# Optimization experiments

Measured on AMD Instinct MI355X. Metric: run time of the kernel, lower is better.

## Reference

```python
import jax, jax.numpy as jnp
import numpy as np

D = 384
K = 16
RADII = (1.0, 2.0, 4.0, 8.0)


def layer_norm(x, g, b, eps=1e-5):
    m = jnp.mean(x, axis=-1, keepdims=True)
    v = jnp.var(x, axis=-1, keepdims=True)
    return (x - m) * jax.lax.rsqrt(v + eps) * g + b


def fps(pos, M):
    # Farthest point sampling: deterministic start at index 0. pos: (N,3) -> (M,) int indices.
    dmin0 = jnp.sum((pos - pos[0]) ** 2, axis=-1)

    def step(dmin, _):
        nxt = jnp.argmax(dmin)
        d = jnp.sum((pos - pos[nxt]) ** 2, axis=-1)
        return jnp.minimum(dmin, d), nxt

    _, rest = jax.lax.scan(step, dmin0, None, length=M - 1)
    return jnp.concatenate([jnp.zeros((1,), rest.dtype), rest])


def sa_stage(x, pos, r, lw, lb, sw, dw, pw1, pb1, pw2, pb2, aw, ab, lg, lbt):
    # One set-abstraction stage for a single point cloud. x:(N,D), pos:(N,3).
    N = x.shape[0]
    M = N // 4  # ratio = 0.25
    idx = fps(pos, M)
    q_pos = pos[idx]  # (M,3)
    # k-nearest neighbors within radius r (radius grouping)
    d2 = jnp.sum((q_pos[:, None, :] - pos[None, :, :]) ** 2, axis=-1)  # (M,N)
    neg_d, nbr = jax.lax.top_k(-d2, K)  # (M,K) nearest sources
    valid = (-neg_d) <= r * r  # (M,K); self point (dist 0) always valid
    # PointTransformerConv
    v = x @ lw + lb        # lin (value path)
    a_src = x @ sw         # lin_src, no bias
    a_dst = x[idx] @ dw    # lin_dst, no bias
    rel = q_pos[:, None, :] - pos[nbr]  # (M,K,3)  pos_i - pos_j
    delta = jax.nn.relu(jax.nn.relu(rel @ pw1 + pb1) @ pw2 + pb2)  # pos_nn, (M,K,D)
    alpha = jax.nn.relu((a_dst[:, None, :] - a_src[nbr] + delta) @ aw + ab)  # attn_nn
    alpha = jnp.where(valid[:, :, None], alpha, -1e30)
    attn = jax.nn.softmax(alpha, axis=1) * valid[:, :, None]  # per-dst, per-channel softmax
    out = jnp.sum(attn * (v[nbr] + delta), axis=1)  # (M,D) weighted aggregation
    return layer_norm(out, lg, lbt), q_pos


def setup_inputs() -> dict:
    key = jax.random.key(0)
    ks = jax.random.split(key, 8)
    B, N = 4, 4096
    s = 0.05
    inp = {"pts": jax.random.normal(ks[0], (B, N, 3 + D), jnp.float32)}
    inp["lin_w"] = jax.random.normal(ks[1], (4, D, D), jnp.float32) * s
    inp["lin_b"] = jnp.zeros((4, D), jnp.float32)
    inp["src_w"] = jax.random.normal(ks[2], (4, D, D), jnp.float32) * s
    inp["dst_w"] = jax.random.normal(ks[3], (4, D, D), jnp.float32) * s
    inp["pos_w1"] = jax.random.normal(ks[4], (4, 3, D), jnp.float32) * s
    inp["pos_b1"] = jnp.zeros((4, D), jnp.float32)
    inp["pos_w2"] = jax.random.normal(ks[5], (4, D, D), jnp.float32) * s
    inp["pos_b2"] = jnp.zeros((4, D), jnp.float32)
    inp["attn_w"] = jax.random.normal(ks[6], (4, D, D), jnp.float32) * s
    inp["attn_b"] = jnp.zeros((4, D), jnp.float32)
    inp["ln_g"] = jnp.ones((4, D), jnp.float32)
    inp["ln_b"] = jnp.zeros((4, D), jnp.float32)
    inp["proj_w"] = jax.random.normal(ks[7], (D, D), jnp.float32) * s
    inp["proj_b"] = jnp.zeros((D,), jnp.float32)
    inp["pln_g"] = jnp.ones((D,), jnp.float32)
    inp["pln_b"] = jnp.zeros((D,), jnp.float32)
    return inp


def reference(pts, lin_w, lin_b, src_w, dst_w, pos_w1, pos_b1, pos_w2, pos_b2,
              attn_w, attn_b, ln_g, ln_b, proj_w, proj_b, pln_g, pln_b):
    pos = pts[..., :3]
    x = pts[..., 3:]  # in_proj is Identity (in_dim == out_dim)
    for s in range(4):
        stage_fn = lambda xx, pp, s=s: sa_stage(
            xx, pp, RADII[s], lin_w[s], lin_b[s], src_w[s], dst_w[s],
            pos_w1[s], pos_b1[s], pos_w2[s], pos_b2[s], attn_w[s], attn_b[s],
            ln_g[s], ln_b[s])
        x, pos = jax.vmap(stage_fn)(x, pos)
    feat = layer_norm(x @ proj_w + proj_b, pln_g, pln_b)
    pad = jnp.zeros(feat.shape[:2], dtype=bool)  # ~pad_mask: all points valid
    return pos, feat, pad
```

## Files before the change

### kernel.cpp

```cpp
#include <hip/hip_runtime.h>
#include <math.h>


using half8 = __attribute__((ext_vector_type(8))) _Float16;
using f32x4 = __attribute__((ext_vector_type(4))) float;

__device__ __forceinline__ float d2f(float ax, float ay, float az,
                                     float bx, float by, float bz)
{
  const float dx = __fsub_rn(ax, bx);
  const float dy = __fsub_rn(ay, by);
  const float dz = __fsub_rn(az, bz);
  return __fadd_rn(__fadd_rn(__fmul_rn(dx, dx), __fmul_rn(dy, dy)),
                   __fmul_rn(dz, dz));
}

template<int CTRL>
__device__ __forceinline__ unsigned dppmax_step(unsigned v)
{
  const unsigned o = (unsigned)__builtin_amdgcn_update_dpp(
      (int)v, (int)v, CTRL, 0xF, 0xF, false);
  return o > v ? o : v;
}
__device__ __forceinline__ unsigned wave_max_bcast(unsigned v)
{
  v = dppmax_step<0x111>(v);
  v = dppmax_step<0x112>(v);
  v = dppmax_step<0x114>(v);
  v = dppmax_step<0x118>(v);
  v = dppmax_step<0x142>(v);
  v = dppmax_step<0x143>(v);
  return (unsigned)__builtin_amdgcn_readlane((int)v, 63);
}

__global__ __launch_bounds__(128) void split_kernel(
    const float* __restrict__ pts, float* __restrict__ pos0, float* __restrict__ x0)
{
  const int n = blockIdx.x;
  const int b = blockIdx.y;
  const float* src = pts + ((long)b * 4096 + n) * 387;
  float* pd = pos0 + ((long)b * 4096 + n) * 3;
  float* xd = x0 + ((long)b * 4096 + n) * 384;
  for (int e = threadIdx.x; e < 387; e += 128) {
    float v = src[e];
    if (e < 3) pd[e] = v; else xd[e - 3] = v;
  }
}

struct TP { const float* src[5]; _Float16* dst; };
__global__ __launch_bounds__(256) void transpose_kernel(TP p)
{
  const int z = blockIdx.z;
  const float* S = p.src[z >> 2] + (long)(z & 3) * 147456;
  _Float16* Dst = p.dst + (long)z * 147456;
  const int k0 = blockIdx.x * 32, n0 = blockIdx.y * 32;
  __shared__ float tile[32][33];
  const int ti = threadIdx.x & 31, tj = threadIdx.x >> 5;
  #pragma unroll
  for (int p8 = 0; p8 < 32; p8 += 8)
    tile[tj + p8][ti] = S[(long)(k0 + tj + p8) * 384 + n0 + ti];
  __syncthreads();
  #pragma unroll
  for (int p8 = 0; p8 < 32; p8 += 8)
    Dst[(long)(n0 + tj + p8) * 384 + k0 + ti] = (_Float16)tile[ti][tj + p8];
}

template<int NPTS, int NTHR>
__global__ __launch_bounds__(NTHR, 1) void fps_kernel(
    const float* __restrict__ pos,
    int* __restrict__ idx_out, float* __restrict__ pos_out)
{
  constexpr int NPT = NPTS / NTHR;
  constexpr int NW = NTHR / 64;
  constexpr int M = NPTS / 4;
  const int b = blockIdx.x;
  pos += (long)b * NPTS * 3; idx_out += (long)b * M; pos_out += (long)b * M * 3;
  const int t = threadIdx.x;

  __shared__ float spx[NPTS], spy[NPTS], spz[NPTS];
  __shared__ unsigned long long s_key[2][NW > 1 ? NW : 1];

  float px[NPT], py[NPT], pz[NPT], dmin[NPT];
  #pragma unroll
  for (int i = 0; i < NPT; i++) {
    const int j = t * NPT + i;
    px[i] = pos[j*3]; py[i] = pos[j*3+1]; pz[i] = pos[j*3+2];
    spx[j] = px[i]; spy[j] = py[i]; spz[j] = pz[i];
  }
  const float sx = pos[0], sy = pos[1], sz = pos[2];
  float bv = 0.f; int bi = 0;
  #pragma unroll
  for (int i = 0; i < NPT; i++) {
    const float dd = d2f(px[i], py[i], pz[i], sx, sy, sz);
    dmin[i] = dd;
    if (i == 0) { bv = dd; bi = 0; }
    else { const bool g = dd > bv; bv = g ? dd : bv; bi = g ? i : bi; }
  }
  if (t == 0) { idx_out[0] = 0; pos_out[0] = sx; pos_out[1] = sy; pos_out[2] = sz; }
  if (NW > 1) __syncthreads();

  for (int m = 1; m < M; ++m) {
    const unsigned myub = __float_as_uint(bv);
    const unsigned wmax = wave_max_bcast(myub);
    const unsigned long long mk = __ballot(myub == wmax);
    const int srclane = __builtin_ctzll(mk);
    const int lbi = __shfl(bi, srclane);
    const int wj = ((t & ~63) + srclane) * NPT + lbi;

    int sel;
    if (NW > 1) {
      const int p = m & 1;
      if ((t & 63) == 0)
        s_key[p][t >> 6] =
            ((unsigned long long)wmax << 32) | (unsigned)(NPTS - 1 - wj);
      __syncthreads();
      unsigned long long kb = s_key[p][0];
      #pragma unroll
      for (int w2 = 1; w2 < NW; w2++) {
        const unsigned long long o = s_key[p][w2];
        if (o > kb) kb = o;
      }
      sel = NPTS - 1 - (int)(kb & 0xFFFFFFFFu);
    } else {
      sel = wj;
    }
    const float qx = spx[sel], qy = spy[sel], qz = spz[sel];
    if (t == 0) { idx_out[m] = sel; pos_out[m*3] = qx; pos_out[m*3+1] = qy; pos_out[m*3+2] = qz; }
    float nbv = 0.f; int nbi = 0;
    #pragma unroll
    for (int i = 0; i < NPT; i++) {
      const float dd = d2f(px[i], py[i], pz[i], qx, qy, qz);
      const float nd = fminf(dmin[i], dd);
      dmin[i] = nd;
      if (i == 0) { nbv = nd; nbi = 0; }
      else { const bool g = nd > nbv; nbv = g ? nd : nbv; nbi = g ? i : nbi; }
    }
    bv = nbv; bi = nbi;
  }
}

template<int C>
__global__ __launch_bounds__(64) void knn_kernel(
    const float* __restrict__ pos, const float* __restrict__ qpos,
    int N, int M, int* __restrict__ nbr, float* __restrict__ vld, float r2)
{
  const int m = blockIdx.x, b = blockIdx.y;
  pos += (long)b * N * 3; qpos += (long)b * M * 3;
  nbr += (long)b * (1024 * 16); vld += (long)b * (1024 * 16);
  const int lane = threadIdx.x;
  const float qx = qpos[m*3], qy = qpos[m*3+1], qz = qpos[m*3+2];
  unsigned long long key[C];
  #pragma unroll
  for (int c = 0; c < C; c++) {
    const int j = c * 64 + lane;
    const float dd = d2f(pos[j*3], pos[j*3+1], pos[j*3+2], qx, qy, qz);
    key[c] = ((unsigned long long)__float_as_uint(dd) << 32) | (unsigned)j;
  }
  unsigned long long prev = 0;
  for (int k = 0; k < 16; k++) {
    unsigned long long best = ~0ull;
    #pragma unroll
    for (int c = 0; c < C; c++) {
      const bool take = (k == 0) || (key[c] > prev);
      if (take && key[c] < best) best = key[c];
    }
    #pragma unroll
    for (int off = 32; off; off >>= 1) {
      const unsigned long long o = __shfl_xor(best, off);
      if (o < best) best = o;
    }
    prev = best;
    if (lane == 0) {
      nbr[m*16+k] = (int)(best & 0xFFFFFFFFu);
      const float dd = __uint_as_float((unsigned)(best >> 32));
      vld[m*16+k] = (dd <= r2) ? 1.0f : 0.0f;
    }
  }
}

struct GemmP {
  const float* A; long sA;
  const _Float16* Wt;
  const float* bias;
  float* C; long sC;
  int R;
  const int* gather; long sG;
  const float* qpos; long sQ;
  const float* pos;  long sP;
  const int* nbr;    long sN;
  const float* pw1;
  const float* pb1;
  const float* adst; long sAD;
  const float* asrc; long sAS;
  int row0;
};

template<int AMODE, bool GATHER, bool BIAS, bool RELU>
__global__ __launch_bounds__(256) void mgemm_kernel(GemmP p)
{
  const int b = blockIdx.z;
  const int rb = blockIdx.x * 64;
  const int cb = blockIdx.y * 64;
  const int t = threadIdx.x;
  const float* A = p.A ? (p.A + (long)b * p.sA) : nullptr;
  float* C = p.C + (long)b * p.sC;
  const int* gat = GATHER ? (p.gather + (long)b * p.sG) : nullptr;
  const int* nbrb = (AMODE != 0) ? (p.nbr + (long)b * p.sN) : nullptr;

  __shared__ _Float16 As[64][40];
  __shared__ _Float16 Bs[64][40];

  const int w = t >> 6, lane = t & 63;
  const int wm = w & 1, wn = w >> 1;
  const int quad = lane >> 4, l16 = lane & 15;

  f32x4 acc[2][2] = {};

  const int sr = t >> 2;
  const int sk = (t & 3) << 3;
  const int ar = rb + sr;

  const float* arow = nullptr;
  const float* adrow = nullptr;
  const float* asrow = nullptr;
  bool avalid = true;
  float rx = 0.f, ry = 0.f, rz = 0.f;
  if (AMODE == 0) {
    avalid = (ar < p.R);
    long srcrow = 0;
    if (avalid) srcrow = GATHER ? (long)gat[ar] : (long)ar;
    arow = A + srcrow * 384;
  } else {
    const int grow = p.row0 + ar;
    const int mq = grow >> 4;
    const int n = nbrb[grow];
    if (AMODE == 1) {
      const float* qposb = p.qpos + (long)b * p.sQ;
      const float* posb = p.pos + (long)b * p.sP;
      rx = qposb[mq*3+0] - posb[n*3+0];
      ry = qposb[mq*3+1] - posb[n*3+1];
      rz = qposb[mq*3+2] - posb[n*3+2];
    } else {
      arow = A + (long)ar * 384;
      adrow = p.adst + (long)b * p.sAD + (long)mq * 384;
      asrow = p.asrc + (long)b * p.sAS + (long)n * 384;
    }
  }

  for (int k0 = 0; k0 < 384; k0 += 32) {
    float a8[8];
    if (AMODE == 0) {
      if (avalid) {
        const float4 u = *(const float4*)(arow + k0 + sk);
        const float4 v = *(const float4*)(arow + k0 + sk + 4);
        a8[0]=u.x; a8[1]=u.y; a8[2]=u.z; a8[3]=u.w;
        a8[4]=v.x; a8[5]=v.y; a8[6]=v.z; a8[7]=v.w;
      } else {
        #pragma unroll
        for (int j = 0; j < 8; j++) a8[j] = 0.f;
      }
    } else if (AMODE == 1) {
      const int kc = k0 + sk;
      const float4 w0a = *(const float4*)(p.pw1 + kc);
      const float4 w0b = *(const float4*)(p.pw1 + kc + 4);
      const float4 w1a = *(const float4*)(p.pw1 + 384 + kc);
      const float4 w1b = *(const float4*)(p.pw1 + 384 + kc + 4);
      const float4 w2a = *(const float4*)(p.pw1 + 768 + kc);
      const float4 w2b = *(const float4*)(p.pw1 + 768 + kc + 4);
      const float4 b1a = *(const float4*)(p.pb1 + kc);
      const float4 b1b = *(const float4*)(p.pb1 + kc + 4);
      a8[0] = fmaxf(rx*w0a.x + ry*w1a.x + rz*w2a.x + b1a.x, 0.f);
      a8[1] = fmaxf(rx*w0a.y + ry*w1a.y + rz*w2a.y + b1a.y, 0.f);
      a8[2] = fmaxf(rx*w0a.z + ry*w1a.z + rz*w2a.z + b1a.z, 0.f);
      a8[3] = fmaxf(rx*w0a.w + ry*w1a.w + rz*w2a.w + b1a.w, 0.f);
      a8[4] = fmaxf(rx*w0b.x + ry*w1b.x + rz*w2b.x + b1b.x, 0.f);
      a8[5] = fmaxf(rx*w0b.y + ry*w1b.y + rz*w2b.y + b1b.y, 0.f);
      a8[6] = fmaxf(rx*w0b.z + ry*w1b.z + rz*w2b.z + b1b.z, 0.f);
      a8[7] = fmaxf(rx*w0b.w + ry*w1b.w + rz*w2b.w + b1b.w, 0.f);
    } else {
      const int kc = k0 + sk;
      const float4 d0 = *(const float4*)(arow + kc);
      const float4 d1 = *(const float4*)(arow + kc + 4);
      const float4 a0 = *(const float4*)(adrow + kc);
      const float4 a1 = *(const float4*)(adrow + kc + 4);
      const float4 s0 = *(const float4*)(asrow + kc);
      const float4 s1 = *(const float4*)(asrow + kc + 4);
      a8[0] = a0.x - s0.x + d0.x; a8[1] = a0.y - s0.y + d0.y;
      a8[2] = a0.z - s0.z + d0.z; a8[3] = a0.w - s0.w + d0.w;
      a8[4] = a1.x - s1.x + d1.x; a8[5] = a1.y - s1.y + d1.y;
      a8[6] = a1.z - s1.z + d1.z; a8[7] = a1.w - s1.w + d1.w;
    }
    const half8 bv = *(const half8*)(p.Wt + (long)(cb + sr) * 384 + k0 + sk);

    __syncthreads();
    half8 av;
    #pragma unroll
    for (int j = 0; j < 8; j++) av[j] = (_Float16)a8[j];
    *(half8*)&As[sr][sk] = av;
    *(half8*)&Bs[sr][sk] = bv;
    __syncthreads();

    const half8 fa0 = *(const half8*)&As[wm*32 + l16][quad*8];
    const half8 fa1 = *(const half8*)&As[wm*32 + 16 + l16][quad*8];
    const half8 fb0 = *(const half8*)&Bs[wn*32 + l16][quad*8];
    const half8 fb1 = *(const half8*)&Bs[wn*32 + 16 + l16][quad*8];
    acc[0][0] = __builtin_amdgcn_mfma_f32_16x16x32_f16(fa0, fb0, acc[0][0], 0, 0, 0);
    acc[0][1] = __builtin_amdgcn_mfma_f32_16x16x32_f16(fa0, fb1, acc[0][1], 0, 0, 0);
    acc[1][0] = __builtin_amdgcn_mfma_f32_16x16x32_f16(fa1, fb0, acc[1][0], 0, 0, 0);
    acc[1][1] = __builtin_amdgcn_mfma_f32_16x16x32_f16(fa1, fb1, acc[1][1], 0, 0, 0);
  }

  float bi0 = 0.f, bi1 = 0.f;
  if (BIAS) {
    bi0 = p.bias[cb + wn*32 + l16];
    bi1 = p.bias[cb + wn*32 + 16 + l16];
  }
  #pragma unroll
  for (int i = 0; i < 2; i++) {
    const int base = rb + wm*32 + i*16;
    if (base < p.R) {
      const int r0 = base + quad*4;
      #pragma unroll
      for (int j = 0; j < 2; j++) {
        const int col = cb + wn*32 + j*16 + l16;
        const float bb = j ? bi1 : bi0;
        #pragma unroll
        for (int reg = 0; reg < 4; reg++) {
          float v = acc[i][j][reg] + bb;
          if (RELU) v = fmaxf(v, 0.f);
          C[(long)(r0 + reg) * 384 + col] = v;
        }
      }
    }
  }
}

__global__ __launch_bounds__(128) void attnln_kernel(
    const float* __restrict__ alpha, const float* __restrict__ delta,
    const float* __restrict__ vbuf, const int* __restrict__ nbr,
    const float* __restrict__ vldb, const float* __restrict__ lng,
    const float* __restrict__ lnb, float* __restrict__ xout,
    int q0, long sCh, long sV, long sNb, long sX)
{
  const int ml = blockIdx.x, b = blockIdx.y;
  const int m = q0 + ml;
  alpha += (long)b * sCh; delta += (long)b * sCh; vbuf += (long)b * sV;
  nbr += (long)b * sNb; vldb += (long)b * sNb; xout += (long)b * sX;
  const int t = threadIdx.x;

  int nb[16]; float vl[16];
  #pragma unroll
  for (int k = 0; k < 16; k++) { nb[k] = nbr[m*16+k]; vl[k] = vldb[m*16+k]; }

  const long rbase = (long)ml * 16 * 384;
  float av[16][3];
  #pragma unroll
  for (int k = 0; k < 16; k++)
    #pragma unroll
    for (int i = 0; i < 3; i++) {
      const float a = alpha[rbase + k*384 + t + i*128];
      av[k][i] = (vl[k] > 0.5f) ? a : -1e30f;
    }
  float mx[3] = {-3.4e38f, -3.4e38f, -3.4e38f};
  #pragma unroll
  for (int k = 0; k < 16; k++)
    #pragma unroll
    for (int i = 0; i < 3; i++) mx[i] = fmaxf(mx[i], av[k][i]);
  float sm[3] = {0.f, 0.f, 0.f};
  #pragma unroll
  for (int k = 0; k < 16; k++)
    #pragma unroll
    for (int i = 0; i < 3; i++) { const float e = expf(av[k][i] - mx[i]); av[k][i] = e; sm[i] += e; }
  float rs[3];
  #pragma unroll
  for (int i = 0; i < 3; i++) rs[i] = 1.0f / sm[i];
  float o[3] = {0.f, 0.f, 0.f};
  #pragma unroll
  for (int k = 0; k < 16; k++) {
    const long nrow = (long)nb[k] * 384;
    #pragma unroll
    for (int i = 0; i < 3; i++) {
      const int dd = t + i * 128;
      const float vv = vbuf[nrow + dd] + delta[rbase + k*384 + dd];
      o[i] += (av[k][i] * rs[i] * vl[k]) * vv;
    }
  }
  __shared__ float sred[2];
  float s1 = o[0] + o[1] + o[2];
  #pragma unroll
  for (int off = 32; off; off >>= 1) s1 += __shfl_xor(s1, off);
  if ((t & 63) == 0) sred[t >> 6] = s1;
  __syncthreads();
  const float mean = (sred[0] + sred[1]) * (1.0f / 384.0f);
  __syncthreads();
  float s2 = 0.f;
  #pragma unroll
  for (int i = 0; i < 3; i++) { const float dd = o[i] - mean; s2 += dd * dd; }
  #pragma unroll
  for (int off = 32; off; off >>= 1) s2 += __shfl_xor(s2, off);
  if ((t & 63) == 0) sred[t >> 6] = s2;
  __syncthreads();
  const float var = (sred[0] + sred[1]) * (1.0f / 384.0f);
  const float rstd = 1.0f / sqrtf(var + 1e-5f);
  #pragma unroll
  for (int i = 0; i < 3; i++) {
    const int dd = t + i * 128;
    xout[(long)m * 384 + dd] = (o[i] - mean) * rstd * lng[dd] + lnb[dd];
  }
}

__global__ __launch_bounds__(384) void feat_kernel(
    const float* __restrict__ x4, const float* __restrict__ pw,
    const float* __restrict__ pb, const float* __restrict__ g,
    const float* __restrict__ be, float* __restrict__ outf)
{
  const int row = blockIdx.x, b = blockIdx.y;
  const long r = (long)b * 16 + row;
  const int d = threadIdx.x;
  __shared__ float xs[384];
  xs[d] = x4[r * 384 + d];
  __syncthreads();
  float acc = pb[d];
  #pragma unroll 8
  for (int j = 0; j < 384; j++) acc = fmaf(xs[j], pw[(long)j * 384 + d], acc);
  __shared__ float sred[6];
  float s = acc;
  #pragma unroll
  for (int off = 32; off; off >>= 1) s += __shfl_xor(s, off);
  if ((d & 63) == 0) sred[d >> 6] = s;
  __syncthreads();
  const float mean = (sred[0]+sred[1]+sred[2]+sred[3]+sred[4]+sred[5]) * (1.0f/384.0f);
  __syncthreads();
  float dv = (acc - mean) * (acc - mean);
  #pragma unroll
  for (int off = 32; off; off >>= 1) dv += __shfl_xor(dv, off);
  if ((d & 63) == 0) sred[d >> 6] = dv;
  __syncthreads();
  const float var = (sred[0]+sred[1]+sred[2]+sred[3]+sred[4]+sred[5]) * (1.0f/384.0f);
  const float rstd = 1.0f / sqrtf(var + 1e-5f);
  outf[r * 384 + d] = (acc - mean) * rstd * g[d] + be[d];
}

__global__ void tail_kernel(const float* __restrict__ p4, float* __restrict__ out)
{
  const int t = threadIdx.x;
  if (t < 192) out[t] = p4[t];
  if (t < 64) out[192 + 24576 + t] = 0.0f;
}

extern "C" void kernel_launch(void* const* d_in, const int* in_sizes, int n_in,
                              void* d_out, int out_size, void* d_ws, size_t ws_size,
                              hipStream_t stream)
{
  (void)in_sizes; (void)n_in; (void)out_size; (void)ws_size;
  const float* pts    = (const float*)d_in[0];
  const float* lin_w  = (const float*)d_in[1];
  const float* lin_b  = (const float*)d_in[2];
  const float* src_w  = (const float*)d_in[3];
  const float* dst_w  = (const float*)d_in[4];
  const float* pos_w1 = (const float*)d_in[5];
  const float* pos_b1 = (const float*)d_in[6];
  const float* pos_w2 = (const float*)d_in[7];
  const float* pos_b2 = (const float*)d_in[8];
  const float* attn_w = (const float*)d_in[9];
  const float* attn_b = (const float*)d_in[10];
  const float* ln_g   = (const float*)d_in[11];
  const float* ln_b   = (const float*)d_in[12];
  const float* proj_w = (const float*)d_in[13];
  const float* proj_b = (const float*)d_in[14];
  const float* pln_g  = (const float*)d_in[15];
  const float* pln_b  = (const float*)d_in[16];
  float* out = (float*)d_out;

  constexpr long SX0 = 4096L*384, SX1 = 1024L*384, SX2 = 256L*384, SX3 = 64L*384, SX4 = 16L*384;
  constexpr long SP0 = 4096L*3, SP1 = 1024L*3, SP2 = 256L*3, SP3 = 64L*3, SP4 = 16L*3;
  constexpr long SV  = 4096L*384;
  constexpr long SAD = 1024L*384;
  constexpr long SCH = 4096L*384;
  constexpr long SNB = 1024L*16;

  _Float16* wt = (_Float16*)d_ws;
  float* ws = (float*)(wt + 20L * 147456);
  float* x0 = ws; ws += 4*SX0;
  float* x1 = ws; ws += 4*SX1;
  float* x2 = ws; ws += 4*SX2;
  float* x3 = ws; ws += 4*SX3;
  float* x4 = ws; ws += 4*SX4;
  float* p0 = ws; ws += 4*SP0;
  float* p1 = ws; ws += 4*SP1;
  float* p2 = ws; ws += 4*SP2;
  float* p3 = ws; ws += 4*SP3;
  float* p4 = ws; ws += 4*SP4;
  float* vb = ws; ws += 4*SV;
  float* asb = ws; ws += 4*SV;
  float* adb = ws; ws += 4*SAD;
  float* db = ws; ws += 4*SCH;
  float* ab = ws; ws += 4*SCH;
  float* vld = ws; ws += 4*SNB;
  int* nb = (int*)ws; ws += 4*SNB;
  int* ix[4];
  ix[0] = (int*)ws; ws += 4*1024;
  ix[1] = (int*)ws; ws += 4*256;
  ix[2] = (int*)ws; ws += 4*64;
  ix[3] = (int*)ws; ws += 4*16;

  const int Ns[4] = {4096, 1024, 256, 64};
  const int Ms[4] = {1024, 256, 64, 16};
  const float R2[4] = {1.0f, 4.0f, 16.0f, 64.0f};
  float* X[5] = {x0, x1, x2, x3, x4};
  float* P[5] = {p0, p1, p2, p3, p4};
  long SPs[5] = {SP0, SP1, SP2, SP3, SP4};
  long SXs[5] = {SX0, SX1, SX2, SX3, SX4};

  split_kernel<<<dim3(4096, 4), 128, 0, stream>>>(pts, p0, x0);

  {
    TP tp{};
    tp.src[0] = lin_w; tp.src[1] = src_w; tp.src[2] = dst_w;
    tp.src[3] = pos_w2; tp.src[4] = attn_w;
    tp.dst = wt;
    transpose_kernel<<<dim3(12, 12, 20), 256, 0, stream>>>(tp);
  }

  fps_kernel<4096, 256><<<dim3(4), 256, 0, stream>>>(P[0], ix[0], P[1]);
  fps_kernel<1024, 256><<<dim3(4), 256, 0, stream>>>(P[1], ix[1], P[2]);
  fps_kernel<256, 64><<<dim3(4), 64, 0, stream>>>(P[2], ix[2], P[3]);
  fps_kernel<64, 64><<<dim3(4), 64, 0, stream>>>(P[3], ix[3], P[4]);

  for (int s = 0; s < 4; s++) {
    const int N = Ns[s], M = Ms[s];
    switch (s) {
      case 0: knn_kernel<64><<<dim3(M, 4), 64, 0, stream>>>(P[s], P[s+1], N, M, nb, vld, R2[s]); break;
      case 1: knn_kernel<16><<<dim3(M, 4), 64, 0, stream>>>(P[s], P[s+1], N, M, nb, vld, R2[s]); break;
      case 2: knn_kernel<4><<<dim3(M, 4), 64, 0, stream>>>(P[s], P[s+1], N, M, nb, vld, R2[s]); break;
      default: knn_kernel<1><<<dim3(M, 4), 64, 0, stream>>>(P[s], P[s+1], N, M, nb, vld, R2[s]); break;
    }
    {
      GemmP g{}; g.A = X[s]; g.sA = SXs[s]; g.Wt = wt + (long)(0*4+s)*147456; g.bias = lin_b + (long)s*384;
      g.C = vb; g.sC = SV; g.R = N;
      mgemm_kernel<0, false, true, false><<<dim3(N/64, 6, 4), 256, 0, stream>>>(g);
    }
    {
      GemmP g{}; g.A = X[s]; g.sA = SXs[s]; g.Wt = wt + (long)(1*4+s)*147456;
      g.C = asb; g.sC = SV; g.R = N;
      mgemm_kernel<0, false, false, false><<<dim3(N/64, 6, 4), 256, 0, stream>>>(g);
    }
    {
      GemmP g{}; g.A = X[s]; g.sA = SXs[s]; g.Wt = wt + (long)(2*4+s)*147456;
      g.C = adb; g.sC = SAD; g.R = M; g.gather = ix[s]; g.sG = M;
      mgemm_kernel<0, true, false, false><<<dim3((M+63)/64, 6, 4), 256, 0, stream>>>(g);
    }
    const int nch = (M + 255) / 256;
    for (int c = 0; c < nch; c++) {
      const int q0 = c * 256;
      const int Mc = (M - q0 < 256) ? (M - q0) : 256;
      const int rows = Mc * 16;
      {
        GemmP g{}; g.Wt = wt + (long)(3*4+s)*147456; g.bias = pos_b2 + (long)s*384;
        g.C = db; g.sC = SCH; g.R = rows;
        g.qpos = P[s+1]; g.sQ = SPs[s+1]; g.pos = P[s]; g.sP = SPs[s];
        g.nbr = nb; g.sN = SNB; g.pw1 = pos_w1 + (long)s*1152; g.pb1 = pos_b1 + (long)s*384;
        g.row0 = q0 * 16;
        mgemm_kernel<1, false, true, true><<<dim3(rows/64, 6, 4), 256, 0, stream>>>(g);
      }
      {
        GemmP g{}; g.A = db; g.sA = SCH; g.Wt = wt + (long)(4*4+s)*147456; g.bias = attn_b + (long)s*384;
        g.C = ab; g.sC = SCH; g.R = rows;
        g.nbr = nb; g.sN = SNB; g.adst = adb; g.sAD = SAD; g.asrc = asb; g.sAS = SV;
        g.row0 = q0 * 16;
        mgemm_kernel<2, false, true, true><<<dim3(rows/64, 6, 4), 256, 0, stream>>>(g);
      }
      attnln_kernel<<<dim3(Mc, 4), 128, 0, stream>>>(
          ab, db, vb, nb, vld, ln_g + (long)s*384, ln_b + (long)s*384,
          X[s+1], q0, SCH, SV, SNB, (long)M*384);
    }
  }

  feat_kernel<<<dim3(16, 4), 384, 0, stream>>>(x4, proj_w, proj_b, pln_g, pln_b, out + 192);
  tail_kernel<<<1, 256, 0, stream>>>(p4, out);
}
```

Before: 1.467 ms.

## Co-schedule stage-0 FPS with value and source GEMMs in one fused launch

The stage-0 farthest-point-sampling kernel and the stage-0 lin and lin_src GEMMs are merged into one launch. Block IDs are split so the first four blocks run FPS and the remaining blocks run GEMM tiles, all sharing one static LDS buffer. The long serial FPS, which occupies only four workgroups, can then overlap with the independent GEMM work instead of leaving the GPU mostly idle. In exchange, every block reserves the larger FPS-sized shared memory, which may limit how many GEMM blocks fit per CU.

New measurement: 1.458 ms. About the same (-0.6%).

```diff
diff --git a/kernel.cpp b/kernel.cpp
--- a/kernel.cpp
+++ b/kernel.cpp
@@ -66,19 +66,17 @@
 }
 
 template<int NPTS, int NTHR>
-__global__ __launch_bounds__(NTHR, 1) void fps_kernel(
+__device__ __forceinline__ void fps_body(
     const float* __restrict__ pos,
-    int* __restrict__ idx_out, float* __restrict__ pos_out)
+    int* __restrict__ idx_out, float* __restrict__ pos_out,
+    int b, int t,
+    float* __restrict__ spx, float* __restrict__ spy, float* __restrict__ spz,
+    unsigned long long* __restrict__ s_key)
 {
   constexpr int NPT = NPTS / NTHR;
   constexpr int NW = NTHR / 64;
   constexpr int M = NPTS / 4;
-  const int b = blockIdx.x;
   pos += (long)b * NPTS * 3; idx_out += (long)b * M; pos_out += (long)b * M * 3;
-  const int t = threadIdx.x;
-
-  __shared__ float spx[NPTS], spy[NPTS], spz[NPTS];
-  __shared__ unsigned long long s_key[2][NW > 1 ? NW : 1];
 
   float px[NPT], py[NPT], pz[NPT], dmin[NPT];
   #pragma unroll
@@ -111,13 +109,13 @@
     if (NW > 1) {
       const int p = m & 1;
       if ((t & 63) == 0)
-        s_key[p][t >> 6] =
+        s_key[p*NW + (t >> 6)] =
             ((unsigned long long)wmax << 32) | (unsigned)(NPTS - 1 - wj);
       __syncthreads();
-      unsigned long long kb = s_key[p][0];
+      unsigned long long kb = s_key[p*NW];
       #pragma unroll
       for (int w2 = 1; w2 < NW; w2++) {
-        const unsigned long long o = s_key[p][w2];
+        const unsigned long long o = s_key[p*NW + w2];
         if (o > kb) kb = o;
       }
       sel = NPTS - 1 - (int)(kb & 0xFFFFFFFFu);
@@ -137,6 +135,17 @@
     }
     bv = nbv; bi = nbi;
   }
+}
+
+template<int NPTS, int NTHR>
+__global__ __launch_bounds__(NTHR, 1) void fps_kernel(
+    const float* __restrict__ pos,
+    int* __restrict__ idx_out, float* __restrict__ pos_out)
+{
+  __shared__ float spx[NPTS], spy[NPTS], spz[NPTS];
+  __shared__ unsigned long long s_key[2 * (NTHR > 64 ? NTHR / 64 : 1)];
+  fps_body<NPTS, NTHR>(pos, idx_out, pos_out, blockIdx.x, threadIdx.x,
+                       spx, spy, spz, s_key);
 }
 
 template<int C>
@@ -195,20 +204,19 @@
   int row0;
 };
 
+typedef _Float16 (*H40)[40];
+
 template<int AMODE, bool GATHER, bool BIAS, bool RELU>
-__global__ __launch_bounds__(256) void mgemm_kernel(GemmP p)
-{
-  const int b = blockIdx.z;
-  const int rb = blockIdx.x * 64;
-  const int cb = blockIdx.y * 64;
-  const int t = threadIdx.x;
+__device__ __forceinline__ void mgemm_body(
+    const GemmP& p, int bx, int by, int bz, int t, H40 As, H40 Bs)
+{
+  const int b = bz;
+  const int rb = bx * 64;
+  const int cb = by * 64;
   const float* A = p.A ? (p.A + (long)b * p.sA) : nullptr;
   float* C = p.C + (long)b * p.sC;
   const int* gat = GATHER ? (p.gather + (long)b * p.sG) : nullptr;
   const int* nbrb = (AMODE != 0) ? (p.nbr + (long)b * p.sN) : nullptr;
-
-  __shared__ _Float16 As[64][40];
-  __shared__ _Float16 Bs[64][40];
 
   const int w = t >> 6, lane = t & 63;
   const int wm = w & 1, wn = w >> 1;
@@ -335,6 +343,39 @@
   }
 }
 
+template<int AMODE, bool GATHER, bool BIAS, bool RELU>
+__global__ __launch_bounds__(256) void mgemm_kernel(GemmP p)
+{
+  __shared__ _Float16 As[64][40];
+  __shared__ _Float16 Bs[64][40];
+  mgemm_body<AMODE, GATHER, BIAS, RELU>(p, blockIdx.x, blockIdx.y, blockIdx.z,
+                                        threadIdx.x, As, Bs);
+}
+
+__global__ __launch_bounds__(256) void fat1_kernel(
+    const float* fpos, int* fidx, float* fpout, GemmP gv, GemmP ga)
+{
+  __shared__ char buf[49664] __attribute__((aligned(16)));
+  int bid = blockIdx.x; const int t = threadIdx.x;
+  if (bid < 4) {
+    float* spx = (float*)buf;
+    float* spy = spx + 4096;
+    float* spz = spy + 4096;
+    unsigned long long* s_key = (unsigned long long*)(spz + 4096);
+    fps_body<4096, 256>(fpos, fidx, fpout, bid, t, spx, spy, spz, s_key);
+    return;
+  }
+  bid -= 4;
+  H40 As = (H40)buf;
+  H40 Bs = (H40)(buf + 64 * 40 * sizeof(_Float16));
+  if (bid < 1536) {
+    mgemm_body<0, false, true, false>(gv, bid & 63, (bid >> 6) % 6, bid / 384, t, As, Bs);
+    return;
+  }
+  bid -= 1536;
+  mgemm_body<0, false, false, false>(ga, bid & 63, (bid >> 6) % 6, bid / 384, t, As, Bs);
+}
+
 __global__ __launch_bounds__(128) void attnln_kernel(
     const float* __restrict__ alpha, const float* __restrict__ delta,
     const float* __restrict__ vbuf, const int* __restrict__ nbr,
@@ -522,7 +563,14 @@
     transpose_kernel<<<dim3(12, 12, 20), 256, 0, stream>>>(tp);
   }
 
-  fps_kernel<4096, 256><<<dim3(4), 256, 0, stream>>>(P[0], ix[0], P[1]);
+  {
+    GemmP gv{}; gv.A = x0; gv.sA = SX0; gv.Wt = wt + (long)(0*4+0)*147456;
+    gv.bias = lin_b; gv.C = vb; gv.sC = SV; gv.R = 4096;
+    GemmP ga{}; ga.A = x0; ga.sA = SX0; ga.Wt = wt + (long)(1*4+0)*147456;
+    ga.C = asb; ga.sC = SV; ga.R = 4096;
+    fat1_kernel<<<dim3(4 + 1536 + 1536), 256, 0, stream>>>(p0, ix[0], p1, gv, ga);
+  }
+
   fps_kernel<1024, 256><<<dim3(4), 256, 0, stream>>>(P[1], ix[1], P[2]);
   fps_kernel<256, 64><<<dim3(4), 64, 0, stream>>>(P[2], ix[2], P[3]);
   fps_kernel<64, 64><<<dim3(4), 64, 0, stream>>>(P[3], ix[3], P[4]);
@@ -535,15 +583,13 @@
       case 2: knn_kernel<4><<<dim3(M, 4), 64, 0, stream>>>(P[s], P[s+1], N, M, nb, vld, R2[s]); break;
       default: knn_kernel<1><<<dim3(M, 4), 64, 0, stream>>>(P[s], P[s+1], N, M, nb, vld, R2[s]); break;
     }
-    {
+    if (s > 0) {
       GemmP g{}; g.A = X[s]; g.sA = SXs[s]; g.Wt = wt + (long)(0*4+s)*147456; g.bias = lin_b + (long)s*384;
       g.C = vb; g.sC = SV; g.R = N;
       mgemm_kernel<0, false, true, false><<<dim3(N/64, 6, 4), 256, 0, stream>>>(g);
-    }
-    {
-      GemmP g{}; g.A = X[s]; g.sA = SXs[s]; g.Wt = wt + (long)(1*4+s)*147456;
-      g.C = asb; g.sC = SV; g.R = N;
-      mgemm_kernel<0, false, false, false><<<dim3(N/64, 6, 4), 256, 0, stream>>>(g);
+      GemmP g2{}; g2.A = X[s]; g2.sA = SXs[s]; g2.Wt = wt + (long)(1*4+s)*147456;
+      g2.C = asb; g2.sC = SV; g2.R = N;
+      mgemm_kernel<0, false, false, false><<<dim3(N/64, 6, 4), 256, 0, stream>>>(g2);
     }
     {
       GemmP g{}; g.A = X[s]; g.sA = SXs[s]; g.Wt = wt + (long)(2*4+s)*147456;
```
